# Kernel optimization log

Measured on AMD Instinct MI355X. Metric: run time of the kernel, lower is better.

The kernel has to match this reference:

```python
import jax, jax.numpy as jnp
import numpy as np

B, T, D, R = 8, 4096, 768, 16
DB = D // 3  # bucket size (d_img = d_sym = 256, d_rf = D - 2*DB = 256)


def setup_inputs() -> dict:
    key = jax.random.key(0)
    ks = jax.random.split(key, 10)
    s = 0.05
    x = jax.random.normal(ks[0], (B, T, D), dtype=jnp.float32)
    # torch nn.Linear stores weight as (out, in); y = x @ W.T + b
    V_w = jax.random.normal(ks[1], (R, D), dtype=jnp.float32) * s
    U_w = jax.random.normal(ks[2], (D, R), dtype=jnp.float32) * s
    E1_w = jax.random.normal(ks[3], (DB, D), dtype=jnp.float32) * s
    E1_b = jnp.zeros((DB,), dtype=jnp.float32)
    E2_w = jax.random.normal(ks[4], (3, DB), dtype=jnp.float32) * s
    E2_b = jnp.zeros((3,), dtype=jnp.float32)
    # a_base init per bucket: img=-0.6, sym=-1.0, rf=-1.6; a_delta init 0 (perturbed so tanh path is exercised)
    a_base = jnp.concatenate([
        jnp.full((DB,), -0.6, dtype=jnp.float32),
        jnp.full((DB,), -1.0, dtype=jnp.float32),
        jnp.full((D - 2 * DB,), -1.6, dtype=jnp.float32),
    ])
    a_delta = jax.random.normal(ks[5], (D,), dtype=jnp.float32) * 0.1
    C_w = jax.random.normal(ks[6], (D, D), dtype=jnp.float32) * s
    G_w = jax.random.normal(ks[7], (D, D), dtype=jnp.float32) * s
    G_b = jnp.zeros((D,), dtype=jnp.float32)
    return {"x": x, "V_w": V_w, "U_w": U_w, "E1_w": E1_w, "E1_b": E1_b,
            "E2_w": E2_w, "E2_b": E2_b, "a_base": a_base, "a_delta": a_delta,
            "C_w": C_w, "G_w": G_w, "G_b": G_b}


def reference(x, V_w, U_w, E1_w, E1_b, E2_w, E2_b, a_base, a_delta, C_w, G_w, G_b):
    d = x.shape[-1]
    db = d // 3
    # Low-rank input projection: Bu = U(V(x))
    Z = jnp.einsum('btd,rd->btr', x, V_w)            # (B,T,R)
    Bu = jnp.einsum('btr,dr->btd', Z, U_w)           # (B,T,D)
    # Evidence scores per timestep (3 clinical buckets)
    h = jax.nn.gelu(jnp.einsum('btd,ed->bte', x, E1_w) + E1_b, approximate=False)
    alpha = jax.nn.sigmoid(jnp.einsum('bte,ce->btc', h, E2_w) + E2_b)  # (B,T,3)
    # Broadcast each bucket's evidence score over its channels
    alpha_rep = jnp.concatenate([
        jnp.broadcast_to(alpha[..., 0:1], alpha.shape[:-1] + (db,)),
        jnp.broadcast_to(alpha[..., 1:2], alpha.shape[:-1] + (db,)),
        jnp.broadcast_to(alpha[..., 2:3], alpha.shape[:-1] + (d - 2 * db,)),
    ], axis=-1)                                       # (B,T,D)
    a_eff = a_base + alpha_rep * jnp.tanh(a_delta)    # (B,T,D)
    lam = jnp.exp(-jax.nn.softplus(-a_eff))           # (B,T,D), in (0,1)
    # Diagonal linear recurrence s_t = lam_t * s_{t-1} + Bu_t  (scan over time)
    def step(s, inp):
        l_t, bu_t = inp
        s = l_t * s + bu_t
        return s, s
    s0 = jnp.zeros(x.shape[:1] + x.shape[2:], dtype=x.dtype)  # (B,D)
    _, S = jax.lax.scan(step, s0, (jnp.swapaxes(lam, 0, 1), jnp.swapaxes(Bu, 0, 1)))
    S = jnp.swapaxes(S, 0, 1)                         # (B,T,D)
    y = jnp.einsum('btd,od->bto', S, C_w)
    gate = jax.nn.sigmoid(jnp.einsum('btd,od->bto', x, G_w) + G_b)
    y = jax.nn.gelu(y, approximate=False) * gate
    return x + y  # dropout is identity in eval mode
```

## Files before the change

kernel.cpp:

```cpp
#include <hip/hip_runtime.h>
#include <hip/hip_bf16.h>
#include <math.h>

#define B_   8
#define T_   4096
#define D_   768
#define R_   16
#define DB_  256
#define N_   (B_ * T_)
#define NC_  64
#define L_   (T_ / NC_)
#define NKS_ (D_ / 32)

typedef __attribute__((ext_vector_type(8))) short bf16x8;
typedef __attribute__((ext_vector_type(4))) float f32x4;

__device__ __forceinline__ float gelu_exact(float x) {
    return 0.5f * x * (1.0f + erff(x * 0.70710678118654752f));
}
__device__ __forceinline__ float sigmoidf_(float x) {
    return 1.0f / (1.0f + expf(-x));
}
__device__ __forceinline__ float bf2f(unsigned short u) {
    return __uint_as_float(((unsigned)u) << 16);
}
__device__ __forceinline__ unsigned short f2bf(float f) {
    __hip_bfloat16 h = __float2bfloat16(f);
    return *(unsigned short*)&h;
}
__device__ __forceinline__ bf16x8 pack8(float4 a, float4 b) {
    bf16x8 r;
    r[0] = (short)f2bf(a.x); r[1] = (short)f2bf(a.y);
    r[2] = (short)f2bf(a.z); r[3] = (short)f2bf(a.w);
    r[4] = (short)f2bf(b.x); r[5] = (short)f2bf(b.y);
    r[6] = (short)f2bf(b.z); r[7] = (short)f2bf(b.w);
    return r;
}

__device__ __forceinline__ void gload16(const unsigned short* g, unsigned short* l) {
    __builtin_amdgcn_global_load_lds(
        (const __attribute__((address_space(1))) unsigned int*)(const void*)g,
        (__attribute__((address_space(3))) unsigned int*)(void*)l,
        16, 0, 0);
}

__device__ __forceinline__ void stage_tile(const unsigned short* src, int ld,
                                           int row0, int k0,
                                           unsigned short* lds, int w, int l) {
#pragma unroll
    for (int j = 0; j < 2; ++j) {
        int i   = ((w * 2 + j) << 6) + l;
        int row = i >> 2;
        int q   = i & 3;
        int qs  = q ^ ((row >> 1) & 3);
        const unsigned short* g = src + (size_t)(row0 + row) * ld + k0 + qs * 8;
        gload16(g, lds + ((w * 2 + j) << 9));
    }
}

__device__ __forceinline__ bf16x8 frag_read(const unsigned short* lds, int row, int lq) {
    int q = lq ^ ((row >> 1) & 3);
    return *(const bf16x8*)(lds + row * 32 + q * 8);
}

__device__ __forceinline__ void tile_mfma(const unsigned short* bc,
                                          int wrow, int wcol, int lr, int lq,
                                          f32x4 acc[4][4]) {
    bf16x8 a[4], b[4];
#pragma unroll
    for (int m = 0; m < 4; m++) a[m] = frag_read(bc, wrow + m * 16 + lr, lq);
#pragma unroll
    for (int n = 0; n < 4; n++) b[n] = frag_read(bc + 4096, wcol + n * 16 + lr, lq);
    __builtin_amdgcn_s_setprio(1);
#pragma unroll
    for (int m = 0; m < 4; m++)
#pragma unroll
        for (int n = 0; n < 4; n++)
            acc[m][n] = __builtin_amdgcn_mfma_f32_16x16x32_bf16(a[m], b[n], acc[m][n], 0, 0, 0);
    __builtin_amdgcn_s_setprio(0);
}

__device__ __forceinline__ void kloop_prologue(const unsigned short* __restrict__ A,
                                               const unsigned short* __restrict__ Bm,
                                               int row0, int col0,
                                               unsigned short* lds, int w, int l) {
    stage_tile(A,  D_, row0, 0,  lds,         w, l);
    stage_tile(Bm, D_, col0, 0,  lds + 4096,  w, l);
    stage_tile(A,  D_, row0, 32, lds + 8192,  w, l);
    stage_tile(Bm, D_, col0, 32, lds + 12288, w, l);
}

template <bool DO_PROLOGUE>
__device__ __forceinline__ void kloop3(const unsigned short* __restrict__ A,
                                       const unsigned short* __restrict__ Bm,
                                       int row0, int col0,
                                       unsigned short* lds,
                                       int w, int l, f32x4 acc[4][4]) {
    const int lr = l & 15, lq = l >> 4;
    const int wrow = (w >> 1) * 64, wcol = (w & 1) * 64;

    if (DO_PROLOGUE) kloop_prologue(A, Bm, row0, col0, lds, w, l);

#pragma unroll 3
    for (int t = 0; t < NKS_ - 2; ++t) {
        asm volatile("s_waitcnt vmcnt(4)" ::: "memory");
        __builtin_amdgcn_s_barrier();
        __builtin_amdgcn_sched_barrier(0);
        unsigned short* bn = lds + ((t + 2) % 3) * 8192;
        stage_tile(A,  D_, row0, (t + 2) * 32, bn,        w, l);
        stage_tile(Bm, D_, col0, (t + 2) * 32, bn + 4096, w, l);
        tile_mfma(lds + (t % 3) * 8192, wrow, wcol, lr, lq, acc);
    }
    asm volatile("s_waitcnt vmcnt(4)" ::: "memory");
    __builtin_amdgcn_s_barrier();
    __builtin_amdgcn_sched_barrier(0);
    tile_mfma(lds + ((NKS_ - 2) % 3) * 8192, wrow, wcol, lr, lq, acc);
    asm volatile("s_waitcnt vmcnt(0)" ::: "memory");
    __builtin_amdgcn_s_barrier();
    __builtin_amdgcn_sched_barrier(0);
    tile_mfma(lds + ((NKS_ - 1) % 3) * 8192, wrow, wcol, lr, lq, acc);
}

__device__ __forceinline__ void tile_decode(int nwg, int ncol, int& rowt, int& colt) {
    int bid = blockIdx.x;
    int cpx = nwg >> 3;
    int swz = (bid & 7) * cpx + (bid >> 3);
    colt = swz % ncol;
    rowt = swz / ncol;
}

__global__ __launch_bounds__(256, 3)
void gemm_e1_mfma(const unsigned short* __restrict__ Xb,
                  const unsigned short* __restrict__ Wb,
                  const float* __restrict__ bias,
                  unsigned short* __restrict__ H) {
    __shared__ unsigned short lds[3 * 8192];
    const int t = threadIdx.x, l = t & 63, w = t >> 6;
    int rowt, colt;
    tile_decode(512, 2, rowt, colt);
    const int row0 = rowt * 128, col0 = colt * 128;
    const int lr = l & 15, lq = l >> 4;
    const int wrow = (w >> 1) * 64, wcol = (w & 1) * 64;
    f32x4 acc[4][4] = {};
    kloop3<true>(Xb, Wb, row0, col0, lds, w, l, acc);
#pragma unroll
    for (int m = 0; m < 4; m++)
#pragma unroll
        for (int n = 0; n < 4; n++) {
            int col = col0 + wcol + n * 16 + lr;
            float bc = bias[col];
#pragma unroll
            for (int r = 0; r < 4; r++) {
                int row = row0 + wrow + m * 16 + lq * 4 + r;
                H[(size_t)row * DB_ + col] = f2bf(gelu_exact(acc[m][n][r] + bc));
            }
        }
}

__global__ __launch_bounds__(256, 3)
void gemm_fused_out(const unsigned short* __restrict__ Xb,
                    const unsigned short* __restrict__ Gwb,
                    const unsigned short* __restrict__ Sb,
                    const unsigned short* __restrict__ Cwb,
                    const float* __restrict__ Gbias,
                    float* __restrict__ out) {
    __shared__ unsigned short lds[3 * 8192];
    const int t = threadIdx.x, l = t & 63, w = t >> 6;
    int rowt, colt;
    tile_decode(1536, 6, rowt, colt);
    const int row0 = rowt * 128, col0 = colt * 128;
    const int lr = l & 15, lq = l >> 4;
    const int wrow = (w >> 1) * 64, wcol = (w & 1) * 64;

    float gb[4];
#pragma unroll
    for (int n = 0; n < 4; n++) gb[n] = Gbias[col0 + wcol + n * 16 + lr];

    f32x4 acc[4][4] = {};
    kloop3<true>(Xb, Gwb, row0, col0, lds, w, l, acc);

    kloop_prologue(Sb, Cwb, row0, col0, lds, w, l);

    unsigned int gp[4][4][2];
#pragma unroll
    for (int m = 0; m < 4; m++)
#pragma unroll
        for (int n = 0; n < 4; n++) {
            gp[m][n][0] = (unsigned)f2bf(sigmoidf_(acc[m][n][0] + gb[n]))
                        | ((unsigned)f2bf(sigmoidf_(acc[m][n][1] + gb[n])) << 16);
            gp[m][n][1] = (unsigned)f2bf(sigmoidf_(acc[m][n][2] + gb[n]))
                        | ((unsigned)f2bf(sigmoidf_(acc[m][n][3] + gb[n])) << 16);
            acc[m][n] = (f32x4){0.f, 0.f, 0.f, 0.f};
        }

    kloop3<false>(Sb, Cwb, row0, col0, lds, w, l, acc);

#pragma unroll
    for (int m = 0; m < 4; m++)
#pragma unroll
        for (int n = 0; n < 4; n++) {
            int col = col0 + wcol + n * 16 + lr;
#pragma unroll
            for (int r = 0; r < 4; r++) {
                int row = row0 + wrow + m * 16 + lq * 4 + r;
                size_t o = (size_t)row * D_ + col;
                float g = bf2f((unsigned short)(gp[m][n][r >> 1] >> ((r & 1) * 16)));
                out[o] = bf2f(Xb[o]) + gelu_exact(acc[m][n][r]) * g;
            }
        }
}

__global__ __launch_bounds__(256)
void cvtz_kernel(const float* __restrict__ X, const float* __restrict__ Vw,
                 unsigned short* __restrict__ Xb, float* __restrict__ Z) {
    const int t = threadIdx.x, l = t & 63, w = t >> 6;
    const int lr = l & 15, lq = l >> 4;
    const int tok0 = (blockIdx.x * 4 + w) * 16;
    const float* xrow = X  + (size_t)(tok0 + lr) * D_;
    const float* vrow = Vw + (size_t)lr * D_;
    f32x4 acc = {};
#pragma unroll 4
    for (int k0 = 0; k0 < D_; k0 += 32) {
        int k = k0 + lq * 8;
        float4 xa = *(const float4*)&xrow[k];
        float4 xb = *(const float4*)&xrow[k + 4];
        float4 va = *(const float4*)&vrow[k];
        float4 vb = *(const float4*)&vrow[k + 4];
        bf16x8 xf = pack8(xa, xb);
        bf16x8 vf = pack8(va, vb);
        *(bf16x8*)&Xb[(size_t)(tok0 + lr) * D_ + k] = xf;
        acc = __builtin_amdgcn_mfma_f32_16x16x32_bf16(xf, vf, acc, 0, 0, 0);
    }
#pragma unroll
    for (int rr = 0; rr < 4; rr++)
        Z[(size_t)(tok0 + lq * 4 + rr) * R_ + lr] = acc[rr];
}

__global__ __launch_bounds__(256)
void alpha_kernel(const unsigned short* __restrict__ H,
                  const float* __restrict__ E2w, const float* __restrict__ E2b,
                  float* __restrict__ alpha) {
    const int t = threadIdx.x, l = t & 63, w = t >> 6;
    const size_t tok = blockIdx.x * 4 + w;
    ushort4 hv = *(const ushort4*)&H[tok * DB_ + l * 4];
    float h0 = bf2f(hv.x), h1 = bf2f(hv.y), h2 = bf2f(hv.z), h3 = bf2f(hv.w);
    float p[3];
#pragma unroll
    for (int c = 0; c < 3; c++) {
        float4 e = *(const float4*)&E2w[c * DB_ + l * 4];
        p[c] = h0 * e.x + h1 * e.y + h2 * e.z + h3 * e.w;
#pragma unroll
        for (int m = 32; m >= 1; m >>= 1) p[c] += __shfl_xor(p[c], m);
    }
    if (l == 0) {
        alpha[tok * 3 + 0] = sigmoidf_(p[0] + E2b[0]);
        alpha[tok * 3 + 1] = sigmoidf_(p[1] + E2b[1]);
        alpha[tok * 3 + 2] = sigmoidf_(p[2] + E2b[2]);
    }
}

__device__ __forceinline__ void load_chunk_lds(const float* __restrict__ Z,
                                               const float* __restrict__ alpha,
                                               int tok0, int t,
                                               float* Zs, float* als) {
#pragma unroll
    for (int i = t; i < L_ * R_ / 4; i += 192)
        *(float4*)&Zs[i * 4] = *(const float4*)&Z[(size_t)tok0 * R_ + i * 4];
    als[t] = alpha[(size_t)tok0 * 3 + t];
}

__device__ __forceinline__ float dot16(const float* zrow, const float4* u) {
    float4 z0 = *(const float4*)&zrow[0],  z1 = *(const float4*)&zrow[4];
    float4 z2 = *(const float4*)&zrow[8],  z3 = *(const float4*)&zrow[12];
    return z0.x*u[0].x + z0.y*u[0].y + z0.z*u[0].z + z0.w*u[0].w
         + z1.x*u[1].x + z1.y*u[1].y + z1.z*u[1].z + z1.w*u[1].w
         + z2.x*u[2].x + z2.y*u[2].y + z2.z*u[2].z + z2.w*u[2].w
         + z3.x*u[3].x + z3.y*u[3].y + z3.z*u[3].z + z3.w*u[3].w;
}

__global__ __launch_bounds__(192)
void scan_pass1(const float* __restrict__ Z, const float* __restrict__ alpha,
                const float* __restrict__ Uw, const float* __restrict__ a_base,
                const float* __restrict__ tanhd,
                float* __restrict__ Aagg, float* __restrict__ Send) {
    __shared__ float Zs[L_ * R_];
    __shared__ float als[L_ * 3];
    const int t = threadIdx.x;
    const int c = blockIdx.x & (NC_ - 1);
    const int b = blockIdx.x >> 6;
    const int tok0 = b * T_ + c * L_;
    const int d0 = t * 4;
    const int buck = d0 >> 8;
    load_chunk_lds(Z, alpha, tok0, t, Zs, als);

    float4 u[4][4];
#pragma unroll
    for (int j = 0; j < 4; j++)
#pragma unroll
        for (int q = 0; q < 4; q++)
            u[j][q] = *(const float4*)&Uw[(size_t)(d0 + j) * R_ + q * 4];
    float4 ab = *(const float4*)&a_base[d0];
    float4 td = *(const float4*)&tanhd[d0];
    float abv[4] = {ab.x, ab.y, ab.z, ab.w};
    float tdv[4] = {td.x, td.y, td.z, td.w};
    __syncthreads();

    float a[4] = {1.f, 1.f, 1.f, 1.f}, s[4] = {};
    for (int i = 0; i < L_; i++) {
        float av = als[i * 3 + buck];
#pragma unroll
        for (int j = 0; j < 4; j++) {
            float lam = sigmoidf_(fmaf(av, tdv[j], abv[j]));
            float bu  = dot16(&Zs[i * R_], u[j]);
            a[j] *= lam;
            s[j] = fmaf(lam, s[j], bu);
        }
    }
    size_t o = ((size_t)(b * NC_ + c)) * D_ + d0;
    *(float4*)&Aagg[o] = make_float4(a[0], a[1], a[2], a[3]);
    *(float4*)&Send[o] = make_float4(s[0], s[1], s[2], s[3]);
}

__global__ void scan_pass2(const float* __restrict__ Aagg, const float* __restrict__ Send,
                           float* __restrict__ Cin) {
    const int d = threadIdx.x;
    const int b = blockIdx.x;
    float s = 0.f;
    for (int c = 0; c < NC_; c++) {
        size_t o = ((size_t)(b * NC_ + c)) * D_ + d;
        Cin[o] = s;
        s = fmaf(Aagg[o], s, Send[o]);
    }
}

__global__ __launch_bounds__(192)
void scan_pass3(const float* __restrict__ Z, const float* __restrict__ alpha,
                const float* __restrict__ Uw, const float* __restrict__ a_base,
                const float* __restrict__ tanhd, const float* __restrict__ Cin,
                unsigned short* __restrict__ Sout) {
    __shared__ float Zs[L_ * R_];
    __shared__ float als[L_ * 3];
    const int t = threadIdx.x;
    const int c = blockIdx.x & (NC_ - 1);
    const int b = blockIdx.x >> 6;
    const int tok0 = b * T_ + c * L_;
    const int d0 = t * 4;
    const int buck = d0 >> 8;
    load_chunk_lds(Z, alpha, tok0, t, Zs, als);

    float4 u[4][4];
#pragma unroll
    for (int j = 0; j < 4; j++)
#pragma unroll
        for (int q = 0; q < 4; q++)
            u[j][q] = *(const float4*)&Uw[(size_t)(d0 + j) * R_ + q * 4];
    float4 ab = *(const float4*)&a_base[d0];
    float4 td = *(const float4*)&tanhd[d0];
    float abv[4] = {ab.x, ab.y, ab.z, ab.w};
    float tdv[4] = {td.x, td.y, td.z, td.w};
    __syncthreads();

    size_t ci = ((size_t)(b * NC_ + c)) * D_ + d0;
    float4 c4 = *(const float4*)&Cin[ci];
    float s[4] = {c4.x, c4.y, c4.z, c4.w};
    for (int i = 0; i < L_; i++) {
        float av = als[i * 3 + buck];
#pragma unroll
        for (int j = 0; j < 4; j++) {
            float lam = sigmoidf_(fmaf(av, tdv[j], abv[j]));
            float bu  = dot16(&Zs[i * R_], u[j]);
            s[j] = fmaf(lam, s[j], bu);
        }
        *(ushort4*)&Sout[(size_t)(tok0 + i) * D_ + d0] =
            make_ushort4(f2bf(s[0]), f2bf(s[1]), f2bf(s[2]), f2bf(s[3]));
    }
}

__global__ void cvt_bf16_vec(const float* __restrict__ in, unsigned short* __restrict__ out, int n4) {
    int i = blockIdx.x * 256 + threadIdx.x;
    if (i < n4) {
        float4 v = ((const float4*)in)[i];
        ((ushort4*)out)[i] = make_ushort4(f2bf(v.x), f2bf(v.y), f2bf(v.z), f2bf(v.w));
    }
}
__global__ void tanh_vec(const float* __restrict__ in, float* __restrict__ out, int n) {
    int i = blockIdx.x * 256 + threadIdx.x;
    if (i < n) out[i] = tanhf(in[i]);
}

extern "C" void kernel_launch(void* const* d_in, const int* in_sizes, int n_in,
                              void* d_out, int out_size, void* d_ws, size_t ws_size,
                              hipStream_t stream) {
    const float* x       = (const float*)d_in[0];
    const float* V_w     = (const float*)d_in[1];
    const float* U_w     = (const float*)d_in[2];
    const float* E1_w    = (const float*)d_in[3];
    const float* E1_b    = (const float*)d_in[4];
    const float* E2_w    = (const float*)d_in[5];
    const float* E2_b    = (const float*)d_in[6];
    const float* a_base  = (const float*)d_in[7];
    const float* a_delta = (const float*)d_in[8];
    const float* C_w     = (const float*)d_in[9];
    const float* G_w     = (const float*)d_in[10];
    const float* G_b     = (const float*)d_in[11];
    float* out = (float*)d_out;

    char* p = (char*)d_ws;
    float* Aagg  = (float*)p;           p += (size_t)B_ * NC_ * D_ * 4;
    float* Send  = (float*)p;           p += (size_t)B_ * NC_ * D_ * 4;
    float* Cin   = (float*)p;           p += (size_t)B_ * NC_ * D_ * 4;
    float* tanhd = (float*)p;           p += (size_t)D_ * 4;
    float* Z     = (float*)p;           p += (size_t)N_ * R_ * 4;
    float* alpha = (float*)p;           p += (size_t)N_ * 3 * 4;
    unsigned short* x_bf  = (unsigned short*)p; p += (size_t)N_ * D_ * 2;
    unsigned short* H_bf  = (unsigned short*)p; p += (size_t)N_ * DB_ * 2;
    unsigned short* S_bf  = (unsigned short*)p; p += (size_t)N_ * D_ * 2;
    unsigned short* E1_bf = (unsigned short*)p; p += (size_t)DB_ * D_ * 2;
    unsigned short* Cw_bf = (unsigned short*)p; p += (size_t)D_ * D_ * 2;
    unsigned short* Gw_bf = (unsigned short*)p; p += (size_t)D_ * D_ * 2;

    {
        int n4 = DB_ * D_ / 4;
        cvt_bf16_vec<<<(n4 + 255) / 256, 256, 0, stream>>>(E1_w, E1_bf, n4);
        n4 = D_ * D_ / 4;
        cvt_bf16_vec<<<(n4 + 255) / 256, 256, 0, stream>>>(C_w, Cw_bf, n4);
        cvt_bf16_vec<<<(n4 + 255) / 256, 256, 0, stream>>>(G_w, Gw_bf, n4);
        tanh_vec<<<3, 256, 0, stream>>>(a_delta, tanhd, D_);
    }

    cvtz_kernel<<<N_ / 64, 256, 0, stream>>>(x, V_w, x_bf, Z);

    gemm_e1_mfma<<<512, 256, 0, stream>>>(x_bf, E1_bf, E1_b, H_bf);
    alpha_kernel<<<N_ / 4, 256, 0, stream>>>(H_bf, E2_w, E2_b, alpha);

    scan_pass1<<<B_ * NC_, 192, 0, stream>>>(Z, alpha, U_w, a_base, tanhd, Aagg, Send);
    scan_pass2<<<B_,       D_,  0, stream>>>(Aagg, Send, Cin);
    scan_pass3<<<B_ * NC_, 192, 0, stream>>>(Z, alpha, U_w, a_base, tanhd, Cin, S_bf);

    gemm_fused_out<<<1536, 256, 0, stream>>>(x_bf, Gw_bf, S_bf, Cw_bf, G_b, out);
}
```

Before: 300.2 us.

## Enlarge GEMM tiles to 256x128 with 8 waves and fuse E2 projection into E1 epilogue

The GEMM kernels move to 512-thread workgroups computing 256x128 output tiles. The A tile is staged by all eight waves and the B tile is shared across them, so each loaded weight tile is reused by twice as many rows. The E1 GEMM epilogue now applies GELU and directly reduces the E2 projection with wave shuffles and atomics. This removes the H intermediate write/read and the separate alpha kernel, at the cost of extra zero and finalize kernels and atomic contention. Occupancy drops to two workgroups per CU and the tile count halves, which may hurt latency hiding or load balance.

Result: no change. 301.6 us (+0.5%).

```diff
diff --git a/kernel.cpp b/kernel.cpp
--- a/kernel.cpp
+++ b/kernel.cpp
@@ -11,6 +11,7 @@
 #define NC_  64
 #define L_   (T_ / NC_)
 #define NKS_ (D_ / 32)
+#define BUF_ 12288
 
 typedef __attribute__((ext_vector_type(8))) short bf16x8;
 typedef __attribute__((ext_vector_type(4))) float f32x4;
@@ -44,18 +45,24 @@
         16, 0, 0);
 }
 
-__device__ __forceinline__ void stage_tile(const unsigned short* src, int ld,
-                                           int row0, int k0,
-                                           unsigned short* lds, int w, int l) {
+__device__ __forceinline__ void stage_a(const unsigned short* src, int row0, int k0,
+                                        unsigned short* lds, int w, int l) {
 #pragma unroll
     for (int j = 0; j < 2; ++j) {
         int i   = ((w * 2 + j) << 6) + l;
         int row = i >> 2;
         int q   = i & 3;
         int qs  = q ^ ((row >> 1) & 3);
-        const unsigned short* g = src + (size_t)(row0 + row) * ld + k0 + qs * 8;
-        gload16(g, lds + ((w * 2 + j) << 9));
-    }
+        gload16(src + (size_t)(row0 + row) * D_ + k0 + qs * 8, lds + ((w * 2 + j) << 9));
+    }
+}
+__device__ __forceinline__ void stage_b(const unsigned short* src, int col0, int k0,
+                                        unsigned short* lds, int w, int l) {
+    int i   = (w << 6) + l;
+    int row = i >> 2;
+    int q   = i & 3;
+    int qs  = q ^ ((row >> 1) & 3);
+    gload16(src + (size_t)(col0 + row) * D_ + k0 + qs * 8, lds + (w << 9));
 }
 
 __device__ __forceinline__ bf16x8 frag_read(const unsigned short* lds, int row, int lq) {
@@ -63,14 +70,14 @@
     return *(const bf16x8*)(lds + row * 32 + q * 8);
 }
 
-__device__ __forceinline__ void tile_mfma(const unsigned short* bc,
+__device__ __forceinline__ void tile_mfma(const unsigned short* la, const unsigned short* lb,
                                           int wrow, int wcol, int lr, int lq,
                                           f32x4 acc[4][4]) {
     bf16x8 a[4], b[4];
 #pragma unroll
-    for (int m = 0; m < 4; m++) a[m] = frag_read(bc, wrow + m * 16 + lr, lq);
-#pragma unroll
-    for (int n = 0; n < 4; n++) b[n] = frag_read(bc + 4096, wcol + n * 16 + lr, lq);
+    for (int m = 0; m < 4; m++) a[m] = frag_read(la, wrow + m * 16 + lr, lq);
+#pragma unroll
+    for (int n = 0; n < 4; n++) b[n] = frag_read(lb, wcol + n * 16 + lr, lq);
     __builtin_amdgcn_s_setprio(1);
 #pragma unroll
     for (int m = 0; m < 4; m++)
@@ -84,10 +91,10 @@
                                                const unsigned short* __restrict__ Bm,
                                                int row0, int col0,
                                                unsigned short* lds, int w, int l) {
-    stage_tile(A,  D_, row0, 0,  lds,         w, l);
-    stage_tile(Bm, D_, col0, 0,  lds + 4096,  w, l);
-    stage_tile(A,  D_, row0, 32, lds + 8192,  w, l);
-    stage_tile(Bm, D_, col0, 32, lds + 12288, w, l);
+    stage_a(A, row0, 0,  lds,                w, l);
+    stage_b(Bm, col0, 0,  lds + 8192,        w, l);
+    stage_a(A, row0, 32, lds + BUF_,         w, l);
+    stage_b(Bm, col0, 32, lds + BUF_ + 8192, w, l);
 }
 
 template <bool DO_PROLOGUE>
@@ -103,22 +110,29 @@
 
 #pragma unroll 3
     for (int t = 0; t < NKS_ - 2; ++t) {
-        asm volatile("s_waitcnt vmcnt(4)" ::: "memory");
+        asm volatile("s_waitcnt vmcnt(3)" ::: "memory");
         __builtin_amdgcn_s_barrier();
         __builtin_amdgcn_sched_barrier(0);
-        unsigned short* bn = lds + ((t + 2) % 3) * 8192;
-        stage_tile(A,  D_, row0, (t + 2) * 32, bn,        w, l);
-        stage_tile(Bm, D_, col0, (t + 2) * 32, bn + 4096, w, l);
-        tile_mfma(lds + (t % 3) * 8192, wrow, wcol, lr, lq, acc);
-    }
-    asm volatile("s_waitcnt vmcnt(4)" ::: "memory");
+        unsigned short* bn = lds + ((t + 2) % 3) * BUF_;
+        stage_a(A, row0, (t + 2) * 32, bn,        w, l);
+        stage_b(Bm, col0, (t + 2) * 32, bn + 8192, w, l);
+        unsigned short* bc = lds + (t % 3) * BUF_;
+        tile_mfma(bc, bc + 8192, wrow, wcol, lr, lq, acc);
+    }
+    asm volatile("s_waitcnt vmcnt(3)" ::: "memory");
     __builtin_amdgcn_s_barrier();
     __builtin_amdgcn_sched_barrier(0);
-    tile_mfma(lds + ((NKS_ - 2) % 3) * 8192, wrow, wcol, lr, lq, acc);
+    {
+        unsigned short* bc = lds + ((NKS_ - 2) % 3) * BUF_;
+        tile_mfma(bc, bc + 8192, wrow, wcol, lr, lq, acc);
+    }
     asm volatile("s_waitcnt vmcnt(0)" ::: "memory");
     __builtin_amdgcn_s_barrier();
     __builtin_amdgcn_sched_barrier(0);
-    tile_mfma(lds + ((NKS_ - 1) % 3) * 8192, wrow, wcol, lr, lq, acc);
+    {
+        unsigned short* bc = lds + ((NKS_ - 1) % 3) * BUF_;
+        tile_mfma(bc, bc + 8192, wrow, wcol, lr, lq, acc);
+    }
 }
 
 __device__ __forceinline__ void tile_decode(int nwg, int ncol, int& rowt, int& colt) {
@@ -129,46 +143,69 @@
     rowt = swz / ncol;
 }
 
-__global__ __launch_bounds__(256, 3)
-void gemm_e1_mfma(const unsigned short* __restrict__ Xb,
-                  const unsigned short* __restrict__ Wb,
-                  const float* __restrict__ bias,
-                  unsigned short* __restrict__ H) {
-    __shared__ unsigned short lds[3 * 8192];
+__global__ __launch_bounds__(512, 2)
+void gemm_e1_alpha(const unsigned short* __restrict__ Xb,
+                   const unsigned short* __restrict__ Wb,
+                   const float* __restrict__ bias,
+                   const float* __restrict__ E2w,
+                   float* __restrict__ alpha_acc) {
+    __shared__ unsigned short lds[3 * BUF_];
     const int t = threadIdx.x, l = t & 63, w = t >> 6;
     int rowt, colt;
-    tile_decode(512, 2, rowt, colt);
-    const int row0 = rowt * 128, col0 = colt * 128;
+    tile_decode(256, 2, rowt, colt);
+    const int row0 = rowt * 256, col0 = colt * 128;
     const int lr = l & 15, lq = l >> 4;
     const int wrow = (w >> 1) * 64, wcol = (w & 1) * 64;
     f32x4 acc[4][4] = {};
     kloop3<true>(Xb, Wb, row0, col0, lds, w, l, acc);
+
+    float bia[4], e2v[3][4];
+#pragma unroll
+    for (int n = 0; n < 4; n++) {
+        int col = col0 + wcol + n * 16 + lr;
+        bia[n] = bias[col];
+#pragma unroll
+        for (int c = 0; c < 3; c++) e2v[c][n] = E2w[c * DB_ + col];
+    }
 #pragma unroll
     for (int m = 0; m < 4; m++)
 #pragma unroll
-        for (int n = 0; n < 4; n++) {
-            int col = col0 + wcol + n * 16 + lr;
-            float bc = bias[col];
-#pragma unroll
-            for (int r = 0; r < 4; r++) {
+        for (int r = 0; r < 4; r++) {
+            float p0 = 0.f, p1 = 0.f, p2 = 0.f;
+#pragma unroll
+            for (int n = 0; n < 4; n++) {
+                float h = gelu_exact(acc[m][n][r] + bia[n]);
+                p0 = fmaf(h, e2v[0][n], p0);
+                p1 = fmaf(h, e2v[1][n], p1);
+                p2 = fmaf(h, e2v[2][n], p2);
+            }
+#pragma unroll
+            for (int s = 1; s < 16; s <<= 1) {
+                p0 += __shfl_xor(p0, s);
+                p1 += __shfl_xor(p1, s);
+                p2 += __shfl_xor(p2, s);
+            }
+            if (lr == 0) {
                 int row = row0 + wrow + m * 16 + lq * 4 + r;
-                H[(size_t)row * DB_ + col] = f2bf(gelu_exact(acc[m][n][r] + bc));
+                atomicAdd(&alpha_acc[(size_t)row * 3 + 0], p0);
+                atomicAdd(&alpha_acc[(size_t)row * 3 + 1], p1);
+                atomicAdd(&alpha_acc[(size_t)row * 3 + 2], p2);
             }
         }
 }
 
-__global__ __launch_bounds__(256, 3)
+__global__ __launch_bounds__(512, 2)
 void gemm_fused_out(const unsigned short* __restrict__ Xb,
                     const unsigned short* __restrict__ Gwb,
                     const unsigned short* __restrict__ Sb,
                     const unsigned short* __restrict__ Cwb,
                     const float* __restrict__ Gbias,
                     float* __restrict__ out) {
-    __shared__ unsigned short lds[3 * 8192];
+    __shared__ unsigned short lds[3 * BUF_];
     const int t = threadIdx.x, l = t & 63, w = t >> 6;
     int rowt, colt;
-    tile_decode(1536, 6, rowt, colt);
-    const int row0 = rowt * 128, col0 = colt * 128;
+    tile_decode(768, 6, rowt, colt);
+    const int row0 = rowt * 256, col0 = colt * 128;
     const int lr = l & 15, lq = l >> 4;
     const int wrow = (w >> 1) * 64, wcol = (w & 1) * 64;
 
@@ -236,27 +273,14 @@
         Z[(size_t)(tok0 + lq * 4 + rr) * R_ + lr] = acc[rr];
 }
 
-__global__ __launch_bounds__(256)
-void alpha_kernel(const unsigned short* __restrict__ H,
-                  const float* __restrict__ E2w, const float* __restrict__ E2b,
-                  float* __restrict__ alpha) {
-    const int t = threadIdx.x, l = t & 63, w = t >> 6;
-    const size_t tok = blockIdx.x * 4 + w;
-    ushort4 hv = *(const ushort4*)&H[tok * DB_ + l * 4];
-    float h0 = bf2f(hv.x), h1 = bf2f(hv.y), h2 = bf2f(hv.z), h3 = bf2f(hv.w);
-    float p[3];
-#pragma unroll
-    for (int c = 0; c < 3; c++) {
-        float4 e = *(const float4*)&E2w[c * DB_ + l * 4];
-        p[c] = h0 * e.x + h1 * e.y + h2 * e.z + h3 * e.w;
-#pragma unroll
-        for (int m = 32; m >= 1; m >>= 1) p[c] += __shfl_xor(p[c], m);
-    }
-    if (l == 0) {
-        alpha[tok * 3 + 0] = sigmoidf_(p[0] + E2b[0]);
-        alpha[tok * 3 + 1] = sigmoidf_(p[1] + E2b[1]);
-        alpha[tok * 3 + 2] = sigmoidf_(p[2] + E2b[2]);
-    }
+__global__ void zero_f32(float* __restrict__ p, int n) {
+    int i = blockIdx.x * 256 + threadIdx.x;
+    if (i < n) p[i] = 0.f;
+}
+__global__ void alpha_fin(const float* __restrict__ acc, const float* __restrict__ E2b,
+                          float* __restrict__ alpha, int n) {
+    int i = blockIdx.x * 256 + threadIdx.x;
+    if (i < n) alpha[i] = sigmoidf_(acc[i] + E2b[i % 3]);
 }
 
 __device__ __forceinline__ void load_chunk_lds(const float* __restrict__ Z,
@@ -406,14 +430,14 @@
     float* out = (float*)d_out;
 
     char* p = (char*)d_ws;
-    float* Aagg  = (float*)p;           p += (size_t)B_ * NC_ * D_ * 4;
-    float* Send  = (float*)p;           p += (size_t)B_ * NC_ * D_ * 4;
-    float* Cin   = (float*)p;           p += (size_t)B_ * NC_ * D_ * 4;
-    float* tanhd = (float*)p;           p += (size_t)D_ * 4;
-    float* Z     = (float*)p;           p += (size_t)N_ * R_ * 4;
-    float* alpha = (float*)p;           p += (size_t)N_ * 3 * 4;
+    float* Aagg   = (float*)p;          p += (size_t)B_ * NC_ * D_ * 4;
+    float* Send   = (float*)p;          p += (size_t)B_ * NC_ * D_ * 4;
+    float* Cin    = (float*)p;          p += (size_t)B_ * NC_ * D_ * 4;
+    float* tanhd  = (float*)p;          p += (size_t)D_ * 4;
+    float* Z      = (float*)p;          p += (size_t)N_ * R_ * 4;
+    float* alpha  = (float*)p;          p += (size_t)N_ * 3 * 4;
+    float* al_acc = (float*)p;          p += (size_t)N_ * 3 * 4;
     unsigned short* x_bf  = (unsigned short*)p; p += (size_t)N_ * D_ * 2;
-    unsigned short* H_bf  = (unsigned short*)p; p += (size_t)N_ * DB_ * 2;
     unsigned short* S_bf  = (unsigned short*)p; p += (size_t)N_ * D_ * 2;
     unsigned short* E1_bf = (unsigned short*)p; p += (size_t)DB_ * D_ * 2;
     unsigned short* Cw_bf = (unsigned short*)p; p += (size_t)D_ * D_ * 2;
@@ -426,16 +450,17 @@
         cvt_bf16_vec<<<(n4 + 255) / 256, 256, 0, stream>>>(C_w, Cw_bf, n4);
         cvt_bf16_vec<<<(n4 + 255) / 256, 256, 0, stream>>>(G_w, Gw_bf, n4);
         tanh_vec<<<3, 256, 0, stream>>>(a_delta, tanhd, D_);
+        zero_f32<<<(N_ * 3 + 255) / 256, 256, 0, stream>>>(al_acc, N_ * 3);
     }
 
     cvtz_kernel<<<N_ / 64, 256, 0, stream>>>(x, V_w, x_bf, Z);
 
-    gemm_e1_mfma<<<512, 256, 0, stream>>>(x_bf, E1_bf, E1_b, H_bf);
-    alpha_kernel<<<N_ / 4, 256, 0, stream>>>(H_bf, E2_w, E2_b, alpha);
+    gemm_e1_alpha<<<256, 512, 0, stream>>>(x_bf, E1_bf, E1_b, E2_w, al_acc);
+    alpha_fin<<<(N_ * 3 + 255) / 256, 256, 0, stream>>>(al_acc, E2_b, alpha, N_ * 3);
 
     scan_pass1<<<B_ * NC_, 192, 0, stream>>>(Z, alpha, U_w, a_base, tanhd, Aagg, Send);
     scan_pass2<<<B_,       D_,  0, stream>>>(Aagg, Send, Cin);
     scan_pass3<<<B_ * NC_, 192, 0, stream>>>(Z, alpha, U_w, a_base, tanhd, Cin, S_bf);
 
-    gemm_fused_out<<<1536, 256, 0, stream>>>(x_bf, Gw_bf, S_bf, Cw_bf, G_b, out);
-}
+    gemm_fused_out<<<768, 512, 0, stream>>>(x_bf, Gw_bf, S_bf, Cw_bf, G_b, out);
+}
```
